# Kernel optimization log

Hardware: AMD Instinct MI355X
Metric: run time of the kernel (lower is better)

The kernel has to match this reference:

```python
import jax, jax.numpy as jnp
import numpy as np

V, E, H, B, S = 50000, 300, 512, 32, 400
SENT_STEP = 20

def _seg_matrix(seq_len, step):
    # PyTorch default: boundaries = range(0, S, step), append S-1 if missing.
    bounds = list(range(0, seq_len, step))
    if bounds[-1] != seq_len - 1:
        bounds.append(seq_len - 1)
    seg = np.searchsorted(np.array(bounds), np.arange(seq_len))  # token -> sentence id
    M = np.zeros((seq_len, len(bounds)), np.float32)
    M[np.arange(seq_len), seg] = 1.0
    M /= M.sum(0, keepdims=True)  # column-normalized -> segment MEAN pooling
    return jnp.asarray(M)

SEG_M = _seg_matrix(S, SENT_STEP)  # [S, n_sent] = [400, 21]

def _gru_dir(x_proj, w_hh, b_hh, reverse):
    # x_proj: [B,T,3H] precomputed x @ W_ih^T + b_ih. PyTorch gate order: r, z, n.
    def step(h, xp):
        gh = h @ w_hh.T + b_hh
        xr, xz, xn = jnp.split(xp, 3, axis=-1)
        hr, hz, hn = jnp.split(gh, 3, axis=-1)
        r = jax.nn.sigmoid(xr + hr)
        z = jax.nn.sigmoid(xz + hz)
        n = jnp.tanh(xn + r * hn)
        h2 = (1.0 - z) * n + z * h
        return h2, h2
    h0 = jnp.zeros((x_proj.shape[0], w_hh.shape[1]), x_proj.dtype)
    h_last, outs = jax.lax.scan(step, h0, x_proj.transpose(1, 0, 2), reverse=reverse)
    return h_last, outs.transpose(1, 0, 2)  # [B,H], [B,T,H]

def _bigru(x, wif, whf, bif, bhf, wib, whb, bib, bhb):
    hf, of = _gru_dir(x @ wif.T + bif, whf, bhf, False)
    hb, ob = _gru_dir(x @ wib.T + bib, whb, bhb, True)
    return jnp.concatenate([of, ob], -1), hf, hb

def setup_inputs():
    key = jax.random.key(0)
    ks = jax.random.split(key, 20)
    f = lambda k, shp: jax.random.normal(k, shp, jnp.float32) * 0.1
    return {
        'input_seq': jax.random.randint(ks[0], (B, S), 0, V),
        'emb': f(ks[1], (V, E)),
        'w_ih_wf': f(ks[2], (3 * H, E)), 'w_hh_wf': f(ks[3], (3 * H, H)),
        'b_ih_wf': f(ks[4], (3 * H,)), 'b_hh_wf': f(ks[5], (3 * H,)),
        'w_ih_wb': f(ks[6], (3 * H, E)), 'w_hh_wb': f(ks[7], (3 * H, H)),
        'b_ih_wb': f(ks[8], (3 * H,)), 'b_hh_wb': f(ks[9], (3 * H,)),
        'w_ih_sf': f(ks[10], (3 * H, 2 * H)), 'w_hh_sf': f(ks[11], (3 * H, H)),
        'b_ih_sf': f(ks[12], (3 * H,)), 'b_hh_sf': f(ks[13], (3 * H,)),
        'w_ih_sb': f(ks[14], (3 * H, 2 * H)), 'w_hh_sb': f(ks[15], (3 * H, H)),
        'b_ih_sb': f(ks[16], (3 * H,)), 'b_hh_sb': f(ks[17], (3 * H,)),
        'fc_w': f(ks[18], (H, 2 * H)), 'fc_b': f(ks[19], (H,)),
    }

def reference(input_seq, emb, w_ih_wf, w_hh_wf, b_ih_wf, b_hh_wf,
              w_ih_wb, w_hh_wb, b_ih_wb, b_hh_wb,
              w_ih_sf, w_hh_sf, b_ih_sf, b_hh_sf,
              w_ih_sb, w_hh_sb, b_ih_sb, b_hh_sb, fc_w, fc_b):
    x = emb[input_seq]  # [B,S,E]; dropout is identity in eval mode
    word_out, _, _ = _bigru(x, w_ih_wf, w_hh_wf, b_ih_wf, b_hh_wf,
                            w_ih_wb, w_hh_wb, b_ih_wb, b_hh_wb)  # [B,S,2H]
    # fused ragged segment-mean pooling (replaces the double python loop)
    sent_rep = jnp.einsum('btd,ts->bsd', word_out, SEG_M)  # [B,n_sent,2H]
    sent_out, hf, hb = _bigru(sent_rep, w_ih_sf, w_hh_sf, b_ih_sf, b_hh_sf,
                              w_ih_sb, w_hh_sb, b_ih_sb, b_hh_sb)
    hidden = jnp.concatenate([hf, hb], -1) @ fc_w.T + fc_b  # [B,H]
    return sent_out, hidden
```

## Files before the change

### kernel.cpp

```cpp
#include <hip/hip_runtime.h>
#include <hip/hip_bf16.h>
#include <hip/hip_cooperative_groups.h>

typedef __bf16 bf16;
typedef __bf16 bf16x4 __attribute__((ext_vector_type(4)));
typedef __bf16 bf16x8 __attribute__((ext_vector_type(8)));
typedef float f32x4 __attribute__((ext_vector_type(4)));

static __device__ __forceinline__ bf16 f2b(float x) { return (bf16)x; }
static __device__ __forceinline__ float b2f(bf16 x) { return (float)x; }

static __device__ __forceinline__ f32x4 mfma16(bf16x8 a, bf16x8 b, f32x4 c) {
  return __builtin_amdgcn_mfma_f32_16x16x32_bf16(a, b, c, 0, 0, 0);
}

static __device__ __forceinline__ bf16x8 loadb8_cc(const bf16* p) {
  bf16x8 v;
  asm volatile("global_load_dwordx4 %0, %1, off sc0 sc1" : "=v"(v) : "v"(p) : "memory");
  return v;
}
static __device__ __forceinline__ void storeb8_cc(bf16* p, bf16x8 v) {
  asm volatile("global_store_dwordx4 %0, %1, off sc0 sc1" :: "v"(p), "v"(v) : "memory");
}

__global__ __launch_bounds__(256) void pad_gather_cvt(
    const float* __restrict__ src, bf16* __restrict__ dst,
    const int* __restrict__ seq, int nrows) {
  int row = blockIdx.x * 4 + (threadIdx.x >> 6);
  int lane = threadIdx.x & 63;
  if (row >= nrows) return;
  int srow;
  if (seq) {
    int s = row >> 5, b = row & 31;
    srow = seq[b * 400 + s];
  } else {
    srow = row;
  }
  const float* sp = src + (size_t)srow * 300;
  bf16* dp = dst + (size_t)row * 320;
  for (int i = lane; i < 320; i += 64) dp[i] = (i < 300) ? f2b(sp[i]) : (bf16)0.f;
}

__global__ __launch_bounds__(256) void cvt_f32_bf16(const float* __restrict__ src,
                                                    bf16* __restrict__ dst,
                                                    int n4) {
  int i = blockIdx.x * 256 + threadIdx.x;
  int stride = gridDim.x * 256;
  for (; i < n4; i += stride) {
    float4 v = ((const float4*)src)[i];
    bf16x4 o = {f2b(v.x), f2b(v.y), f2b(v.z), f2b(v.w)};
    *(bf16x4*)(dst + (size_t)i * 4) = o;
  }
}

__global__ __launch_bounds__(256) void gemm_bt_al(const float* __restrict__ A,
                                                  const bf16* __restrict__ W,
                                                  const float* __restrict__ bias,
                                                  float* __restrict__ C,
                                                  int M, int N, int K) {
  __shared__ bf16 AsH[128][72];
  __shared__ bf16 AsL[128][72];
  __shared__ bf16 Ws[128][72];
  const int n0 = blockIdx.x * 128, m0 = blockIdx.y * 128;
  const int tid = threadIdx.x;
  const int wave = tid >> 6, lane = tid & 63;
  const int l15 = lane & 15, lq = lane >> 4;
  const int wm = (wave >> 1) * 64, wn = (wave & 1) * 64;

  f32x4 acc[4][4] = {};

  for (int k0 = 0; k0 < K; k0 += 64) {
    __syncthreads();
#pragma unroll
    for (int i = 0; i < 8; ++i) {
      int c = tid + 256 * i;
      int r = c >> 4, cc = (c & 15) * 4;
      int gr = m0 + r;
      float4 v = {0.f, 0.f, 0.f, 0.f};
      if (gr < M) v = *(const float4*)(A + (size_t)gr * K + k0 + cc);
      float vv[4] = {v.x, v.y, v.z, v.w};
#pragma unroll
      for (int j = 0; j < 4; ++j) {
        bf16 h = f2b(vv[j]);
        AsH[r][cc + j] = h;
        AsL[r][cc + j] = f2b(vv[j] - b2f(h));
      }
    }
#pragma unroll
    for (int i = 0; i < 4; ++i) {
      int c = tid + 256 * i;
      int r = c >> 3, cc = (c & 7) * 8;
      *(bf16x8*)&Ws[r][cc] = *(const bf16x8*)(W + (size_t)(n0 + r) * K + k0 + cc);
    }
    __syncthreads();
#pragma unroll
    for (int ks = 0; ks < 64; ks += 32) {
      bf16x8 afH[4], afL[4], bfr[4];
#pragma unroll
      for (int i = 0; i < 4; ++i) {
        afH[i] = *(const bf16x8*)&AsH[wm + i * 16 + l15][ks + lq * 8];
        afL[i] = *(const bf16x8*)&AsL[wm + i * 16 + l15][ks + lq * 8];
      }
#pragma unroll
      for (int j = 0; j < 4; ++j)
        bfr[j] = *(const bf16x8*)&Ws[wn + j * 16 + l15][ks + lq * 8];
#pragma unroll
      for (int i = 0; i < 4; ++i)
#pragma unroll
        for (int j = 0; j < 4; ++j) {
          acc[i][j] = mfma16(afH[i], bfr[j], acc[i][j]);
          acc[i][j] = mfma16(afL[i], bfr[j], acc[i][j]);
        }
    }
  }

#pragma unroll
  for (int i = 0; i < 4; ++i)
#pragma unroll
    for (int j = 0; j < 4; ++j) {
      int col = n0 + wn + j * 16 + l15;
      float bv = bias[col];
#pragma unroll
      for (int r = 0; r < 4; ++r) {
        int row = m0 + wm + i * 16 + lq * 4 + r;
        if (row < M) C[(size_t)row * N + col] = acc[i][j][r] + bv;
      }
    }
}

__global__ __launch_bounds__(256) void gru_word(
    const float* __restrict__ whhF, const float* __restrict__ whhB,
    const float* __restrict__ bhhF, const float* __restrict__ bhhB,
    const float* __restrict__ bihF, const float* __restrict__ bihB,
    const bf16* __restrict__ wpad,
    const bf16* __restrict__ xpad,
    bf16* __restrict__ hexb,
    unsigned* __restrict__ flags,
    float* __restrict__ srep)
{
  __shared__ bf16 WlH[48][516];
  __shared__ bf16 WlL[48][516];
  __shared__ bf16 Xw[48][324];
  __shared__ float red[2][4][64][4];
  __shared__ __align__(16) bf16 stg[2][32][16];
  const int tid = threadIdx.x;
  const int bx = blockIdx.x;
  const int dir = bx >> 5, nb = bx & 31;
  const int c0 = nb * 16;
  const float* whh = dir ? whhB : whhF;
  const float* bhh = dir ? bhhB : bhhF;
  const float* bih = dir ? bihB : bihF;
  const bf16* wih = wpad + (size_t)dir * 1536 * 320;
  unsigned* flg = flags + dir * 32;

#pragma unroll
  for (int i = 0; i < 24; ++i) {
    int c = tid + 256 * i;
    int r = c >> 7, kc = (c & 127) * 4;
    int gr = ((r >> 4) << 9) + c0 + (r & 15);
    float4 v = *(const float4*)(whh + (size_t)gr * 512 + kc);
    float vv[4] = {v.x, v.y, v.z, v.w};
#pragma unroll
    for (int j = 0; j < 4; ++j) {
      bf16 h = f2b(vv[j]);
      WlH[r][kc + j] = h;
      WlL[r][kc + j] = f2b(vv[j] - b2f(h));
    }
  }
#pragma unroll
  for (int i = 0; i < 8; ++i) {
    int c = tid + 256 * i;
    if (c < 1920) {
      int r = c / 40, ch = (c % 40) * 8;
      int gr = ((r >> 4) << 9) + c0 + (r & 15);
      *(bf16x8*)&Xw[r][ch] = *(const bf16x8*)(wih + (size_t)gr * 320 + ch);
    }
  }
  __syncthreads();

  const int wave = tid >> 6, lane = tid & 63;
  const int kh = wave >> 1;
  const int mh = wave & 1;
  const int m0 = mh * 16;
  const int l15 = lane & 15, lq = lane >> 4;
  const int colg = c0 + l15;
  const int rowq = m0 + lq * 4;
  const int arow = m0 + l15;
  const int nboff = lq >> 1;
  const int coff = (lq & 1) * 8;
  const float bhr = bhh[colg];
  const float bhz = bhh[512 + colg];
  const float bhn = bhh[1024 + colg];
  const float bir = bih[colg];
  const float biz = bih[512 + colg];
  const float bin_ = bih[1024 + colg];

  float pacc0 = 0.f, pacc1 = 0.f, pacc2 = 0.f, pacc3 = 0.f;
  float hp_reg[4] = {0.f, 0.f, 0.f, 0.f};
  bf16* hex_d = hexb + (size_t)dir * 32768 * 2;

  for (int it = 0; it < 400; ++it) {
    const int t = dir ? (399 - it) : it;
    f32x4 accR = {}, accZ = {}, xN = {}, hN = {};

    {
      const bf16* xrow = xpad + (size_t)(t * 32 + arow) * 320;
      const int kb = kh * 160;
#pragma unroll
      for (int k0 = 0; k0 < 160; k0 += 32) {
        const int kk = kb + k0 + lq * 8;
        bf16x8 a = *(const bf16x8*)(xrow + kk);
        accR = mfma16(a, *(const bf16x8*)&Xw[l15][kk], accR);
        accZ = mfma16(a, *(const bf16x8*)&Xw[16 + l15][kk], accZ);
        xN = mfma16(a, *(const bf16x8*)&Xw[32 + l15][kk], xN);
      }
    }

    if (it > 0) {
      if (tid < 32) {
        while (__hip_atomic_load(&flg[tid], __ATOMIC_RELAXED,
                                 __HIP_MEMORY_SCOPE_AGENT) < (unsigned)it)
          __builtin_amdgcn_s_sleep(1);
      }
      __syncthreads();

      const bf16* hb = hex_d + (size_t)((it - 1) & 1) * 32768;
      const int inrow = arow * 16 + coff;
      bf16x8 hiA[8], loA[8];
#pragma unroll
      for (int c = 0; c < 8; ++c) {
        const bf16* ph = hb + (size_t)(kh * 16 + c * 2 + nboff) * 1024 + inrow;
        hiA[c] = loadb8_cc(ph);
        loA[c] = loadb8_cc(ph + 512);
      }
      asm volatile("s_waitcnt vmcnt(0)" ::: "memory");
      __builtin_amdgcn_sched_barrier(0);

#pragma unroll
      for (int c = 0; c < 8; ++c) {
        const int kk = kh * 256 + c * 32 + lq * 8;
        bf16x8 wrh = *(const bf16x8*)&WlH[l15][kk];
        bf16x8 wrl = *(const bf16x8*)&WlL[l15][kk];
        bf16x8 wzh = *(const bf16x8*)&WlH[16 + l15][kk];
        bf16x8 wzl = *(const bf16x8*)&WlL[16 + l15][kk];
        bf16x8 wnh = *(const bf16x8*)&WlH[32 + l15][kk];
        bf16x8 wnl = *(const bf16x8*)&WlL[32 + l15][kk];
        accR = mfma16(hiA[c], wrh, accR);
        accR = mfma16(loA[c], wrh, accR);
        accR = mfma16(hiA[c], wrl, accR);
        accZ = mfma16(hiA[c], wzh, accZ);
        accZ = mfma16(loA[c], wzh, accZ);
        accZ = mfma16(hiA[c], wzl, accZ);
        hN = mfma16(hiA[c], wnh, hN);
        hN = mfma16(loA[c], wnh, hN);
        hN = mfma16(hiA[c], wnl, hN);
      }
    }

    if (kh == 0) {
      *(f32x4*)&red[mh][0][lane][0] = accR;
      *(f32x4*)&red[mh][1][lane][0] = accZ;
      *(f32x4*)&red[mh][2][lane][0] = xN;
      *(f32x4*)&red[mh][3][lane][0] = hN;
    }
    __syncthreads();
    if (kh == 1) {
      accR = accR + *(const f32x4*)&red[mh][0][lane][0];
      accZ = accZ + *(const f32x4*)&red[mh][1][lane][0];
      xN = xN + *(const f32x4*)&red[mh][2][lane][0];
      hN = hN + *(const f32x4*)&red[mh][3][lane][0];

      float h2v[4];
#pragma unroll
      for (int r = 0; r < 4; ++r) {
        int b = rowq + r;
        float rr = 1.f / (1.f + expf(-(accR[r] + bir + bhr)));
        float zz = 1.f / (1.f + expf(-(accZ[r] + biz + bhz)));
        float nn = tanhf(xN[r] + bin_ + rr * (hN[r] + bhn));
        h2v[r] = (1.f - zz) * nn + zz * hp_reg[r];
        hp_reg[r] = h2v[r];
        bf16 hi = f2b(h2v[r]);
        stg[0][b][l15] = hi;
        stg[1][b][l15] = f2b(h2v[r] - b2f(hi));
      }

      int sg = (t == 0) ? 0 : ((t + 19) / 20);
      if (sg > 20) sg = 20;
      float ic = (sg == 0) ? 1.0f : (sg == 20 ? (1.0f / 19.0f) : 0.05f);
      pacc0 += h2v[0] * ic; pacc1 += h2v[1] * ic;
      pacc2 += h2v[2] * ic; pacc3 += h2v[3] * ic;
      bool flush = dir ? (t == 0 || (t % 20) == 1) : ((t % 20) == 0 || t == 399);
      if (flush) {
        float* sp = srep + ((size_t)(sg * 32 + rowq) * 1024) + (dir << 9) + colg;
        sp[0] = pacc0; sp[1024] = pacc1;
        sp[2048] = pacc2; sp[3072] = pacc3;
        pacc0 = pacc1 = pacc2 = pacc3 = 0.f;
      }
    }

    __syncthreads();
    if (tid < 128) {
      bf16* dst = hex_d + (size_t)(it & 1) * 32768 + (size_t)nb * 1024;
      storeb8_cc(dst + tid * 8, ((const bf16x8*)&stg[0][0][0])[tid]);
    }
    asm volatile("s_waitcnt vmcnt(0)" ::: "memory");
    __syncthreads();
    if (tid == 0)
      __hip_atomic_store(&flg[nb], (unsigned)(it + 1), __ATOMIC_RELAXED,
                         __HIP_MEMORY_SCOPE_AGENT);
  }
}

__global__ __launch_bounds__(256) void gru_sent(
    const float* __restrict__ whhF, const float* __restrict__ whhB,
    const float* __restrict__ bhhF, const float* __restrict__ bhhB,
    const float* __restrict__ xproj,
    bf16* __restrict__ hexb,
    unsigned* __restrict__ flags,
    float* __restrict__ out,
    float* __restrict__ hfin)
{
  __shared__ bf16 WlH[48][516];
  __shared__ bf16 WlL[48][516];
  __shared__ float red[2][3][64][4];
  __shared__ __align__(16) bf16 stg[2][32][16];
  const int tid = threadIdx.x;
  const int bx = blockIdx.x;
  const int dir = bx >> 5, nb = bx & 31;
  const int c0 = nb * 16;
  const float* whh = dir ? whhB : whhF;
  const float* bhh = dir ? bhhB : bhhF;
  unsigned* flg = flags + dir * 32;

#pragma unroll
  for (int i = 0; i < 24; ++i) {
    int c = tid + 256 * i;
    int r = c >> 7, kc = (c & 127) * 4;
    int gr = ((r >> 4) << 9) + c0 + (r & 15);
    float4 v = *(const float4*)(whh + (size_t)gr * 512 + kc);
    float vv[4] = {v.x, v.y, v.z, v.w};
#pragma unroll
    for (int j = 0; j < 4; ++j) {
      bf16 h = f2b(vv[j]);
      WlH[r][kc + j] = h;
      WlL[r][kc + j] = f2b(vv[j] - b2f(h));
    }
  }
  __syncthreads();

  const int wave = tid >> 6, lane = tid & 63;
  const int kh = wave >> 1;
  const int mh = wave & 1;
  const int m0 = mh * 16;
  const int l15 = lane & 15, lq = lane >> 4;
  const int colg = c0 + l15;
  const int rowq = m0 + lq * 4;
  const int arow = m0 + l15;
  const int nboff = lq >> 1;
  const int coff = (lq & 1) * 8;
  const float bhr = bhh[colg];
  const float bhz = bhh[512 + colg];
  const float bhn = bhh[1024 + colg];

  float hp_reg[4] = {0.f, 0.f, 0.f, 0.f};
  bf16* hex_d = hexb + (size_t)dir * 32768 * 2;

  for (int it = 0; it < 21; ++it) {
    const int t = dir ? (20 - it) : it;
    f32x4 accR = {}, accZ = {}, hN = {};

    if (it > 0) {
      if (tid < 32) {
        while (__hip_atomic_load(&flg[tid], __ATOMIC_RELAXED,
                                 __HIP_MEMORY_SCOPE_AGENT) < (unsigned)it)
          __builtin_amdgcn_s_sleep(1);
      }
      __syncthreads();

      const bf16* hb = hex_d + (size_t)((it - 1) & 1) * 32768;
      const int inrow = arow * 16 + coff;
      bf16x8 hiA[8], loA[8];
#pragma unroll
      for (int c = 0; c < 8; ++c) {
        const bf16* ph = hb + (size_t)(kh * 16 + c * 2 + nboff) * 1024 + inrow;
        hiA[c] = loadb8_cc(ph);
        loA[c] = loadb8_cc(ph + 512);
      }
      asm volatile("s_waitcnt vmcnt(0)" ::: "memory");
      __builtin_amdgcn_sched_barrier(0);

#pragma unroll
      for (int c = 0; c < 8; ++c) {
        const int kk = kh * 256 + c * 32 + lq * 8;
        bf16x8 wrh = *(const bf16x8*)&WlH[l15][kk];
        bf16x8 wrl = *(const bf16x8*)&WlL[l15][kk];
        bf16x8 wzh = *(const bf16x8*)&WlH[16 + l15][kk];
        bf16x8 wzl = *(const bf16x8*)&WlL[16 + l15][kk];
        bf16x8 wnh = *(const bf16x8*)&WlH[32 + l15][kk];
        bf16x8 wnl = *(const bf16x8*)&WlL[32 + l15][kk];
        accR = mfma16(hiA[c], wrh, accR);
        accR = mfma16(loA[c], wrh, accR);
        accR = mfma16(hiA[c], wrl, accR);
        accZ = mfma16(hiA[c], wzh, accZ);
        accZ = mfma16(loA[c], wzh, accZ);
        accZ = mfma16(hiA[c], wzl, accZ);
        hN = mfma16(hiA[c], wnh, hN);
        hN = mfma16(loA[c], wnh, hN);
        hN = mfma16(hiA[c], wnl, hN);
      }
    }

    if (kh == 0) {
      *(f32x4*)&red[mh][0][lane][0] = accR;
      *(f32x4*)&red[mh][1][lane][0] = accZ;
      *(f32x4*)&red[mh][2][lane][0] = hN;
    }
    __syncthreads();
    if (kh == 1) {
      accR = accR + *(const f32x4*)&red[mh][0][lane][0];
      accZ = accZ + *(const f32x4*)&red[mh][1][lane][0];
      hN = hN + *(const f32x4*)&red[mh][2][lane][0];

      const float* xp = xproj + ((size_t)dir * 672 + t * 32) * 1536;
#pragma unroll
      for (int r = 0; r < 4; ++r) {
        int b = rowq + r;
        float xr = xp[b * 1536 + colg];
        float xz = xp[b * 1536 + 512 + colg];
        float xn = xp[b * 1536 + 1024 + colg];
        float rr = 1.f / (1.f + expf(-(xr + accR[r] + bhr)));
        float zz = 1.f / (1.f + expf(-(xz + accZ[r] + bhz)));
        float nn = tanhf(xn + rr * (hN[r] + bhn));
        float h2 = (1.f - zz) * nn + zz * hp_reg[r];
        hp_reg[r] = h2;
        bf16 hi = f2b(h2);
        stg[0][b][l15] = hi;
        stg[1][b][l15] = f2b(h2 - b2f(hi));
        out[(size_t)b * (21 * 1024) + (size_t)t * 1024 + (dir << 9) + colg] = h2;
        if (it == 20) hfin[(dir << 14) + b * 512 + colg] = h2;
      }
    }

    __syncthreads();
    if (tid < 128) {
      bf16* dst = hex_d + (size_t)(it & 1) * 32768 + (size_t)nb * 1024;
      storeb8_cc(dst + tid * 8, ((const bf16x8*)&stg[0][0][0])[tid]);
    }
    asm volatile("s_waitcnt vmcnt(0)" ::: "memory");
    __syncthreads();
    if (tid == 0)
      __hip_atomic_store(&flg[nb], (unsigned)(it + 1), __ATOMIC_RELAXED,
                         __HIP_MEMORY_SCOPE_AGENT);
  }
}

__global__ __launch_bounds__(256) void fc_k(const float* __restrict__ hfin,
                                            const float* __restrict__ fcw,
                                            const float* __restrict__ fcb,
                                            float* __restrict__ out) {
  __shared__ float hl[1024];
  int b = blockIdx.x, tid = threadIdx.x;
  for (int i = tid; i < 512; i += 256) {
    hl[i] = hfin[b * 512 + i];
    hl[512 + i] = hfin[16384 + b * 512 + i];
  }
  __syncthreads();
  for (int j = tid; j < 512; j += 256) {
    const float* wr = fcw + (size_t)j * 1024;
    float acc = 0.f;
    for (int k = 0; k < 1024; k += 4) {
      float4 wv = *(const float4*)(wr + k);
      acc += hl[k] * wv.x + hl[k + 1] * wv.y + hl[k + 2] * wv.z +
             hl[k + 3] * wv.w;
    }
    out[688128 + b * 512 + j] = acc + fcb[j];
  }
}

extern "C" void kernel_launch(void* const* d_in, const int* in_sizes, int n_in,
                              void* d_out, int out_size, void* d_ws,
                              size_t ws_size, hipStream_t stream) {
  const int* seq = (const int*)d_in[0];
  const float* emb = (const float*)d_in[1];
  const float* w_ih_wf = (const float*)d_in[2];
  const float* w_hh_wf = (const float*)d_in[3];
  const float* b_ih_wf = (const float*)d_in[4];
  const float* b_hh_wf = (const float*)d_in[5];
  const float* w_ih_wb = (const float*)d_in[6];
  const float* w_hh_wb = (const float*)d_in[7];
  const float* b_ih_wb = (const float*)d_in[8];
  const float* b_hh_wb = (const float*)d_in[9];
  const float* w_ih_sf = (const float*)d_in[10];
  const float* w_hh_sf = (const float*)d_in[11];
  const float* b_ih_sf = (const float*)d_in[12];
  const float* b_hh_sf = (const float*)d_in[13];
  const float* w_ih_sb = (const float*)d_in[14];
  const float* w_hh_sb = (const float*)d_in[15];
  const float* b_ih_sb = (const float*)d_in[16];
  const float* b_hh_sb = (const float*)d_in[17];
  const float* fc_w = (const float*)d_in[18];
  const float* fc_b = (const float*)d_in[19];

  char* ws = (char*)d_ws;
  bf16* xpad = (bf16*)(ws + 0);
  bf16* wpadw = (bf16*)(ws + 8192000);
  bf16* wihs = (bf16*)(ws + 10158080);
  float* srep = (float*)(ws + 16449536);
  float* xps = (float*)(ws + 19202048);
  bf16* hexb = (bf16*)(ws + 27459584);
  float* hfin = (float*)(ws + 27721728);
  unsigned* flags = (unsigned*)(ws + 27852800);

  hipMemsetAsync(ws + 16449536, 0, 27854848 - 16449536, stream);

  pad_gather_cvt<<<3200, 256, 0, stream>>>(emb, xpad, seq, 12800);
  pad_gather_cvt<<<384, 256, 0, stream>>>(w_ih_wf, wpadw, nullptr, 1536);
  pad_gather_cvt<<<384, 256, 0, stream>>>(w_ih_wb, wpadw + 1536 * 320, nullptr,
                                          1536);
  cvt_f32_bf16<<<1536, 256, 0, stream>>>(w_ih_sf, wihs, 393216);
  cvt_f32_bf16<<<1536, 256, 0, stream>>>(w_ih_sb, wihs + 1572864, 393216);

  {
    unsigned* flgW = flags;
    void* args[] = {(void*)&w_hh_wf, (void*)&w_hh_wb, (void*)&b_hh_wf,
                    (void*)&b_hh_wb, (void*)&b_ih_wf, (void*)&b_ih_wb,
                    (void*)&wpadw,   (void*)&xpad,    (void*)&hexb,
                    (void*)&flgW,    (void*)&srep};
    hipLaunchCooperativeKernel((const void*)gru_word, dim3(64), dim3(256),
                               args, 0, stream);
  }

  dim3 g2(12, 6);
  gemm_bt_al<<<g2, 256, 0, stream>>>(srep, wihs, b_ih_sf, xps, 672, 1536, 1024);
  gemm_bt_al<<<g2, 256, 0, stream>>>(srep, wihs + 1572864, b_ih_sb,
                                     xps + (size_t)672 * 1536, 672, 1536, 1024);

  {
    unsigned* flgS = flags + 128;
    float* outp = (float*)d_out;
    const float* xpsc = xps;
    void* args[] = {(void*)&w_hh_sf, (void*)&w_hh_sb, (void*)&b_hh_sf,
                    (void*)&b_hh_sb, (void*)&xpsc,    (void*)&hexb,
                    (void*)&flgS,    (void*)&outp,    (void*)&hfin};
    hipLaunchCooperativeKernel((const void*)gru_sent, dim3(64), dim3(256),
                               args, 0, stream);
  }

  fc_k<<<32, 256, 0, stream>>>(hfin, fc_w, fc_b, (float*)d_out);
}
```

Before: 2.309 ms.

## Fuse sentence weight conversion into merged GEMM and prefetch hidden state earlier

The separate f32-to-bf16 conversion kernels for the sentence input weights are removed. The sentence projection GEMM now reads fp32 weights and converts them while staging into shared memory, and both directions run in a single launch using a z grid dimension. The large workspace memset is cut down to just the flag region. In the word GRU loop, the flag spin-wait and the loads of the previous hidden state are moved ahead of the input-projection MFMAs, so those loads are in flight during that compute. In exchange, the input-projection work no longer overlaps the wait on other blocks. Dropping the memset is only correct if srep and hfin are fully overwritten rather than accumulated into.

```diff
diff --git a/kernel.cpp b/kernel.cpp
--- a/kernel.cpp
+++ b/kernel.cpp
@@ -41,26 +41,18 @@
   for (int i = lane; i < 320; i += 64) dp[i] = (i < 300) ? f2b(sp[i]) : (bf16)0.f;
 }
 
-__global__ __launch_bounds__(256) void cvt_f32_bf16(const float* __restrict__ src,
-                                                    bf16* __restrict__ dst,
-                                                    int n4) {
-  int i = blockIdx.x * 256 + threadIdx.x;
-  int stride = gridDim.x * 256;
-  for (; i < n4; i += stride) {
-    float4 v = ((const float4*)src)[i];
-    bf16x4 o = {f2b(v.x), f2b(v.y), f2b(v.z), f2b(v.w)};
-    *(bf16x4*)(dst + (size_t)i * 4) = o;
-  }
-}
-
-__global__ __launch_bounds__(256) void gemm_bt_al(const float* __restrict__ A,
-                                                  const bf16* __restrict__ W,
-                                                  const float* __restrict__ bias,
-                                                  float* __restrict__ C,
-                                                  int M, int N, int K) {
+__global__ __launch_bounds__(256) void gemm_bt_al2(
+    const float* __restrict__ A, const float* __restrict__ WF,
+    const float* __restrict__ WB, const float* __restrict__ biasF,
+    const float* __restrict__ biasB, float* __restrict__ C,
+    int M, int N, int K) {
   __shared__ bf16 AsH[128][72];
   __shared__ bf16 AsL[128][72];
   __shared__ bf16 Ws[128][72];
+  const int z = blockIdx.z;
+  const float* W = z ? WB : WF;
+  const float* bias = z ? biasB : biasF;
+  float* Cz = C + (size_t)z * M * N;
   const int n0 = blockIdx.x * 128, m0 = blockIdx.y * 128;
   const int tid = threadIdx.x;
   const int wave = tid >> 6, lane = tid & 63;
@@ -87,10 +79,14 @@
       }
     }
 #pragma unroll
-    for (int i = 0; i < 4; ++i) {
+    for (int i = 0; i < 8; ++i) {
       int c = tid + 256 * i;
-      int r = c >> 3, cc = (c & 7) * 8;
-      *(bf16x8*)&Ws[r][cc] = *(const bf16x8*)(W + (size_t)(n0 + r) * K + k0 + cc);
+      int r = c >> 4, cc = (c & 15) * 4;
+      float4 v = *(const float4*)(W + (size_t)(n0 + r) * K + k0 + cc);
+      Ws[r][cc + 0] = f2b(v.x);
+      Ws[r][cc + 1] = f2b(v.y);
+      Ws[r][cc + 2] = f2b(v.z);
+      Ws[r][cc + 3] = f2b(v.w);
     }
     __syncthreads();
 #pragma unroll
@@ -123,7 +119,7 @@
 #pragma unroll
       for (int r = 0; r < 4; ++r) {
         int row = m0 + wm + i * 16 + lq * 4 + r;
-        if (row < M) C[(size_t)row * N + col] = acc[i][j][r] + bv;
+        if (row < M) Cz[(size_t)row * N + col] = acc[i][j][r] + bv;
       }
     }
 }
@@ -188,6 +184,7 @@
   const int arow = m0 + l15;
   const int nboff = lq >> 1;
   const int coff = (lq & 1) * 8;
+  const int kb = kh * 160;
   const float bhr = bhh[colg];
   const float bhz = bhh[512 + colg];
   const float bhn = bhh[1024 + colg];
@@ -203,9 +200,27 @@
     const int t = dir ? (399 - it) : it;
     f32x4 accR = {}, accZ = {}, xN = {}, hN = {};
 
+    bf16x8 hiA[8], loA[8];
+    if (it > 0) {
+      if (tid < 32) {
+        while (__hip_atomic_load(&flg[tid], __ATOMIC_RELAXED,
+                                 __HIP_MEMORY_SCOPE_AGENT) < (unsigned)it)
+          __builtin_amdgcn_s_sleep(1);
+      }
+      __syncthreads();
+
+      const bf16* hb = hex_d + (size_t)((it - 1) & 1) * 32768;
+      const int inrow = arow * 16 + coff;
+#pragma unroll
+      for (int c = 0; c < 8; ++c) {
+        const bf16* ph = hb + (size_t)(kh * 16 + c * 2 + nboff) * 1024 + inrow;
+        hiA[c] = loadb8_cc(ph);
+        loA[c] = loadb8_cc(ph + 512);
+      }
+    }
+
     {
       const bf16* xrow = xpad + (size_t)(t * 32 + arow) * 320;
-      const int kb = kh * 160;
 #pragma unroll
       for (int k0 = 0; k0 < 160; k0 += 32) {
         const int kk = kb + k0 + lq * 8;
@@ -217,25 +232,8 @@
     }
 
     if (it > 0) {
-      if (tid < 32) {
-        while (__hip_atomic_load(&flg[tid], __ATOMIC_RELAXED,
-                                 __HIP_MEMORY_SCOPE_AGENT) < (unsigned)it)
-          __builtin_amdgcn_s_sleep(1);
-      }
-      __syncthreads();
-
-      const bf16* hb = hex_d + (size_t)((it - 1) & 1) * 32768;
-      const int inrow = arow * 16 + coff;
-      bf16x8 hiA[8], loA[8];
-#pragma unroll
-      for (int c = 0; c < 8; ++c) {
-        const bf16* ph = hb + (size_t)(kh * 16 + c * 2 + nboff) * 1024 + inrow;
-        hiA[c] = loadb8_cc(ph);
-        loA[c] = loadb8_cc(ph + 512);
-      }
       asm volatile("s_waitcnt vmcnt(0)" ::: "memory");
       __builtin_amdgcn_sched_barrier(0);
-
 #pragma unroll
       for (int c = 0; c < 8; ++c) {
         const int kk = kh * 256 + c * 32 + lq * 8;
@@ -504,21 +502,18 @@
   char* ws = (char*)d_ws;
   bf16* xpad = (bf16*)(ws + 0);
   bf16* wpadw = (bf16*)(ws + 8192000);
-  bf16* wihs = (bf16*)(ws + 10158080);
   float* srep = (float*)(ws + 16449536);
   float* xps = (float*)(ws + 19202048);
   bf16* hexb = (bf16*)(ws + 27459584);
   float* hfin = (float*)(ws + 27721728);
   unsigned* flags = (unsigned*)(ws + 27852800);
 
-  hipMemsetAsync(ws + 16449536, 0, 27854848 - 16449536, stream);
+  hipMemsetAsync(flags, 0, 2048, stream);
 
   pad_gather_cvt<<<3200, 256, 0, stream>>>(emb, xpad, seq, 12800);
   pad_gather_cvt<<<384, 256, 0, stream>>>(w_ih_wf, wpadw, nullptr, 1536);
   pad_gather_cvt<<<384, 256, 0, stream>>>(w_ih_wb, wpadw + 1536 * 320, nullptr,
                                           1536);
-  cvt_f32_bf16<<<1536, 256, 0, stream>>>(w_ih_sf, wihs, 393216);
-  cvt_f32_bf16<<<1536, 256, 0, stream>>>(w_ih_sb, wihs + 1572864, 393216);
 
   {
     unsigned* flgW = flags;
@@ -530,10 +525,9 @@
                                args, 0, stream);
   }
 
-  dim3 g2(12, 6);
-  gemm_bt_al<<<g2, 256, 0, stream>>>(srep, wihs, b_ih_sf, xps, 672, 1536, 1024);
-  gemm_bt_al<<<g2, 256, 0, stream>>>(srep, wihs + 1572864, b_ih_sb,
-                                     xps + (size_t)672 * 1536, 672, 1536, 1024);
+  dim3 g2(12, 6, 2);
+  gemm_bt_al2<<<g2, 256, 0, stream>>>(srep, w_ih_sf, w_ih_sb, b_ih_sf,
+                                      b_ih_sb, xps, 672, 1536, 1024);
 
   {
     unsigned* flgS = flags + 128;
```

Result: slower. 2.499 ms (+8.2%).
